# Performance work log

Hardware: AMD Instinct MI355X
Metric: run time of the kernel (lower is better)

Reference implementation:

```python
import jax, jax.numpy as jnp
import numpy as np

D_MODEL = 128; N_HEADS = 8; N_LEVELS = 1; N_POINTS = 8
MAX_RES = 10.0
B, H_SP, W_SP = 8, 64, 64


def setup_inputs() -> dict:
    key = jax.random.key(0)
    ks = jax.random.split(key, 8)
    s = 0.02
    f32 = jnp.float32
    return {
        "nbr_fea": jax.random.normal(ks[0], (B, D_MODEL, H_SP, W_SP), f32),
        "ext_fea": jax.random.normal(ks[1], (B, D_MODEL, H_SP, W_SP), f32),
        "W_val": jax.random.normal(ks[2], (D_MODEL, D_MODEL), f32) * s,
        "b_val": jnp.zeros((D_MODEL,), f32),
        "W_off": jax.random.normal(ks[3], (D_MODEL, N_HEADS * N_LEVELS * N_POINTS * 2), f32) * s,
        "b_off": jax.random.normal(ks[4], (N_HEADS * N_LEVELS * N_POINTS * 2,), f32) * s,
        "W_attn": jax.random.normal(ks[5], (D_MODEL, N_HEADS * N_LEVELS * N_POINTS), f32) * s,
        "b_attn": jnp.zeros((N_HEADS * N_LEVELS * N_POINTS,), f32),
        "W_out": jax.random.normal(ks[6], (D_MODEL, D_MODEL), f32) * s,
        "b_out": jnp.zeros((D_MODEL,), f32),
    }


def _deform_attn_align(nbr_fea, ext_fea, W_val, b_val, W_off, b_off, W_attn, b_attn, W_out, b_out):
    b, c, h, w = nbr_fea.shape
    L = h * w
    dh = c // N_HEADS
    # flatten b c h w -> b (h w) c
    query = jnp.transpose(ext_fea, (0, 2, 3, 1)).reshape(b, L, c)
    vin = jnp.transpose(nbr_fea, (0, 2, 3, 1)).reshape(b, L, c)

    # value projection (mask is all-False -> no masked fill needed)
    value = (vin @ W_val + b_val).reshape(b, L, N_HEADS, dh)
    vh = jnp.transpose(value, (0, 2, 1, 3))  # [b, H, L, dh]

    # sampling offsets, clamped by max_residue_magnitude * tanh
    off = MAX_RES * jnp.tanh(query @ W_off + b_off)
    off = off.reshape(b, L, N_HEADS, N_POINTS, 2)  # single level
    attn = jax.nn.softmax((query @ W_attn + b_attn).reshape(b, L, N_HEADS, N_POINTS), axis=-1)

    # reference points in [0,1]; valid_ratio == 1 since padding mask is all-False
    yy, xx = jnp.meshgrid(jnp.arange(h, dtype=jnp.float32), jnp.arange(w, dtype=jnp.float32), indexing="ij")
    ref = jnp.stack([(xx.reshape(-1) + 0.5) / w, (yy.reshape(-1) + 0.5) / h], axis=-1)  # [L, 2]
    norm = jnp.array([w, h], jnp.float32)  # offset_normalizer [W, H]
    loc = ref[None, :, None, None, :] + off / norm  # [b, L, H, P, 2]

    # grid_sample(align_corners=False, padding_mode='zeros') pixel coordinates
    px = jnp.transpose(loc[..., 0] * w - 0.5, (0, 2, 1, 3))  # [b, H, L, P]
    py = jnp.transpose(loc[..., 1] * h - 0.5, (0, 2, 1, 3))

    x0 = jnp.floor(px); y0 = jnp.floor(py)
    fx = px - x0; fy = py - y0
    x0i = x0.astype(jnp.int32); y0i = y0.astype(jnp.int32)

    def gather(xi, yi):
        valid = (xi >= 0) & (xi < w) & (yi >= 0) & (yi < h)
        idx = jnp.clip(yi, 0, h - 1) * w + jnp.clip(xi, 0, w - 1)  # [b, H, L, P]
        g = jnp.take_along_axis(vh, idx.reshape(b, N_HEADS, L * N_POINTS)[..., None], axis=2)
        return g.reshape(b, N_HEADS, L, N_POINTS, dh) * valid[..., None]

    samp = (gather(x0i, y0i) * ((1.0 - fx) * (1.0 - fy))[..., None]
            + gather(x0i + 1, y0i) * (fx * (1.0 - fy))[..., None]
            + gather(x0i, y0i + 1) * ((1.0 - fx) * fy)[..., None]
            + gather(x0i + 1, y0i + 1) * (fx * fy)[..., None])  # [b, H, L, P, dh]

    aw = jnp.transpose(attn, (0, 2, 1, 3))  # [b, H, L, P]
    out = jnp.sum(samp * aw[..., None], axis=3)  # [b, H, L, dh]
    out = jnp.transpose(out, (0, 2, 1, 3)).reshape(b, L, c)
    out = out @ W_out + b_out
    return jnp.transpose(out.reshape(b, h, w, c), (0, 3, 1, 2))  # b c h w


def reference(nbr_fea, ext_fea, W_val, b_val, W_off, b_off, W_attn, b_attn, W_out, b_out):
    return _deform_attn_align(nbr_fea, ext_fea, W_val, b_val, W_off, b_off, W_attn, b_attn, W_out, b_out)
```

## Files before the change

kernel.cpp:

```cpp
#include <hip/hip_runtime.h>
#include <cstdint>

#define HB 8
#define CM 128
#define NHEAD 8
#define NPT 8
#define DHD 16
#define HS 64
#define WS 64
#define LTOT 4096
#define NQA 192

typedef float floatx4 __attribute__((ext_vector_type(4)));
typedef short bf16x8 __attribute__((ext_vector_type(8)));

__device__ __forceinline__ unsigned short f2bf_rne(float x) {
  unsigned u = __float_as_uint(x);
  return (unsigned short)((u + 0x7FFFu + ((u >> 16) & 1)) >> 16);
}
__device__ __forceinline__ void split_bf(float x, unsigned short& h, unsigned short& l) {
  unsigned u = __float_as_uint(x);
  h = (unsigned short)(u >> 16);
  float r = x - __uint_as_float(u & 0xFFFF0000u);
  l = (unsigned short)(__float_as_uint(r) >> 16);
}
__device__ __forceinline__ float fast_tanh(float x) {
  float e = __expf(2.0f * x);
  return 1.0f - 2.0f / (e + 1.0f);
}

__global__ __launch_bounds__(256) void prep(const float* __restrict__ Wv,
                                            const float* __restrict__ Wo,
                                            const float* __restrict__ Wa,
                                            const float* __restrict__ Ww,
                                            const float* __restrict__ bo,
                                            const float* __restrict__ ba,
                                            unsigned short* __restrict__ wf_val,
                                            unsigned short* __restrict__ wf_qa,
                                            unsigned short* __restrict__ wf_out,
                                            float* __restrict__ bias_qa) {
  const int gid = blockIdx.x * 256 + threadIdx.x;
  const int k4 = gid / 448;
  const int ng = gid - k4 * 448;

  const float* src;
  unsigned short* dst;
  int Nsrc, Nn, nd, n;
  if (ng < 128) {        src = Wv; dst = wf_val; Nsrc = 128; Nn = 128; n = ng;        nd = n; }
  else if (ng < 256) {   src = Wo; dst = wf_qa;  Nsrc = 128; Nn = 192; n = ng - 128;  nd = n; }
  else if (ng < 320) {   src = Wa; dst = wf_qa;  Nsrc = 64;  Nn = 192; n = ng - 256;  nd = n + 128; }
  else {                 src = Ww; dst = wf_out; Nsrc = 128; Nn = 128; n = ng - 320;  nd = n; }

  ushort4 hi, lo;
  split_bf(src[(k4 * 4 + 0) * Nsrc + n], hi.x, lo.x);
  split_bf(src[(k4 * 4 + 1) * Nsrc + n], hi.y, lo.y);
  split_bf(src[(k4 * 4 + 2) * Nsrc + n], hi.z, lo.z);
  split_bf(src[(k4 * 4 + 3) * Nsrc + n], hi.w, lo.w);
  const int off = (k4 >> 1) * Nn * 8 + nd * 8 + (k4 & 1) * 4;
  *(ushort4*)(dst + off) = hi;
  *(ushort4*)(dst + Nn * 128 + off) = lo;

  if (gid < 128) bias_qa[gid] = bo[gid];
  else if (gid < 192) bias_qa[gid] = ba[gid - 128];
}

template <int N, int AMODE, int OUT_MODE>
__global__ __launch_bounds__(256, 4) void gemm_mfma(const void* __restrict__ Av,
                                                    const unsigned short* __restrict__ WF,
                                                    const float* __restrict__ bias,
                                                    float* __restrict__ out) {
  __shared__ char smem[32768];
  unsigned short* AB = (unsigned short*)smem;
  const int t = threadIdx.x;
  const int ml0 = blockIdx.x * 64;
  const int nb0 = blockIdx.y * 64;
  const int b = blockIdx.z;
  const int w = t >> 6, lane = t & 63;
  const int wm = (w >> 1) * 32, wn = (w & 1) * 32;
  const int nl = lane & 15, q = lane >> 4;

  bf16x8 wh[2][4], wl[2][4];
#pragma unroll
  for (int nt = 0; nt < 2; nt++) {
    const int n = nb0 + wn + nt * 16 + nl;
#pragma unroll
    for (int K0 = 0; K0 < 4; K0++) {
      const size_t o = (size_t)(K0 * 4 + q) * N * 8 + n * 8;
      wh[nt][K0] = *(const bf16x8*)(WF + o);
      wl[nt][K0] = *(const bf16x8*)(WF + (size_t)N * 128 + o);
    }
  }

  if (AMODE == 0) {
    const float* src = (const float*)Av + (size_t)b * CM * LTOT + ml0;
    const int x = t & 63, kq = t >> 6;
#pragma unroll
    for (int i = 0; i < 8; i++) {
      const int kb = kq * 4 + i * 16;
      ushort4 hi, lo;
      split_bf(src[(size_t)(kb + 0) * LTOT + x], hi.x, lo.x);
      split_bf(src[(size_t)(kb + 1) * LTOT + x], hi.y, lo.y);
      split_bf(src[(size_t)(kb + 2) * LTOT + x], hi.z, lo.z);
      split_bf(src[(size_t)(kb + 3) * LTOT + x], hi.w, lo.w);
      const int off = x * 128 + (((kb >> 3) ^ (x & 15)) << 3) + (kb & 7);
      *(ushort4*)(AB + off) = hi;
      *(ushort4*)(AB + 8192 + off) = lo;
    }
  } else {
    const unsigned short* src = (const unsigned short*)Av + ((size_t)b * LTOT + ml0) * CM;
#pragma unroll
    for (int i = 0; i < 4; i++) {
      const int idx = t + i * 256;
      const int x = idx >> 4, kc = idx & 15;
      const uint4 v = *(const uint4*)(src + (size_t)x * CM + kc * 8);
      *(uint4*)(AB + x * 128 + ((kc ^ (x & 15)) << 3)) = v;
    }
  }
  __syncthreads();

  floatx4 acc[2][2];
#pragma unroll
  for (int mt = 0; mt < 2; mt++)
#pragma unroll
    for (int nt = 0; nt < 2; nt++) acc[mt][nt] = {0.0f, 0.0f, 0.0f, 0.0f};

#pragma unroll
  for (int K0 = 0; K0 < 4; K0++) {
    bf16x8 ah[2], al[2];
#pragma unroll
    for (int mt = 0; mt < 2; mt++) {
      const int m = wm + mt * 16 + nl;
      const int off = m * 128 + (((K0 * 4 + q) ^ (m & 15)) << 3);
      ah[mt] = *(bf16x8*)(AB + off);
      if (AMODE == 0) al[mt] = *(bf16x8*)(AB + 8192 + off);
    }
#pragma unroll
    for (int mt = 0; mt < 2; mt++)
#pragma unroll
      for (int nt = 0; nt < 2; nt++) {
        if (AMODE == 0)
          acc[mt][nt] = __builtin_amdgcn_mfma_f32_16x16x32_bf16(al[mt], wh[nt][K0], acc[mt][nt], 0, 0, 0);
        acc[mt][nt] = __builtin_amdgcn_mfma_f32_16x16x32_bf16(ah[mt], wl[nt][K0], acc[mt][nt], 0, 0, 0);
        acc[mt][nt] = __builtin_amdgcn_mfma_f32_16x16x32_bf16(ah[mt], wh[nt][K0], acc[mt][nt], 0, 0, 0);
      }
  }

  if (OUT_MODE == 2) {
    __syncthreads();
    float* LF = (float*)smem;
#pragma unroll
    for (int mt = 0; mt < 2; mt++)
#pragma unroll
      for (int nt = 0; nt < 2; nt++) {
        const int n = wn + nt * 16 + nl;
#pragma unroll
        for (int r = 0; r < 4; r++) LF[n * 65 + wm + mt * 16 + q * 4 + r] = acc[mt][nt][r];
      }
    __syncthreads();
#pragma unroll
    for (int i = 0; i < 16; i++) {
      const int idx = t + i * 256;
      const int n = idx >> 6, m = idx & 63;
      out[((size_t)b * CM + nb0 + n) * LTOT + ml0 + m] = LF[n * 65 + m] + bias[nb0 + n];
    }
  } else {
#pragma unroll
    for (int nt = 0; nt < 2; nt++) {
      const int gc = nb0 + wn + nt * 16 + nl;
      const float bv = bias[gc];
#pragma unroll
      for (int mt = 0; mt < 2; mt++)
#pragma unroll
        for (int r = 0; r < 4; r++) {
          const int m = ml0 + wm + mt * 16 + q * 4 + r;
          const float v = acc[mt][nt][r] + bv;
          if (OUT_MODE == 0)
            out[(((size_t)b * NHEAD + (gc >> 4)) * LTOT + m) * DHD + (gc & 15)] = v;
          else
            out[((size_t)b * LTOT + m) * N + gc] = v;
        }
    }
  }
}

__global__ __launch_bounds__(256) void sampler(const float* __restrict__ value,
                                               const float* __restrict__ qa,
                                               unsigned short* __restrict__ attout) {
  const int t = threadIdx.x;
  const int lane = t & 63;
  const int w = t >> 6;
  const int d4 = lane & 3;
  const int p = (lane >> 2) & 7;
  const int li = lane >> 5;
  const int h = blockIdx.y;
  const int b = blockIdx.z;
  const int l = blockIdx.x * 8 + w * 2 + li;
  const size_t bl = (size_t)b * LTOT + l;

  const float2 off2 = *(const float2*)(qa + bl * NQA + h * 16 + p * 2);
  const float logit = qa[bl * NQA + 128 + h * 8 + p];

  float m = logit;
  m = fmaxf(m, __shfl_xor(m, 4));
  m = fmaxf(m, __shfl_xor(m, 8));
  m = fmaxf(m, __shfl_xor(m, 16));
  const float e = __expf(logit - m);
  float s = e;
  s += __shfl_xor(s, 4);
  s += __shfl_xor(s, 8);
  s += __shfl_xor(s, 16);
  const float aw = e / s;

  const float px = (float)(l & (WS - 1)) + 10.0f * fast_tanh(off2.x);
  const float py = (float)(l >> 6) + 10.0f * fast_tanh(off2.y);
  const float x0f = floorf(px), y0f = floorf(py);
  const float fx = px - x0f, fy = py - y0f;
  const int ix = (int)x0f, iy = (int)y0f;

  const float* vb = value + ((size_t)b * NHEAD + h) * (LTOT * DHD) + d4 * 4;
  float4 o = {0.0f, 0.0f, 0.0f, 0.0f};
#pragma unroll
  for (int c = 0; c < 4; c++) {
    const int cdx = c & 1, cdy = c >> 1;
    const int jx = ix + cdx, jy = iy + cdy;
    const float wx = cdx ? fx : 1.0f - fx;
    const float wy = cdy ? fy : 1.0f - fy;
    const bool valid = ((unsigned)jx < WS) & ((unsigned)jy < HS);
    const float wc = valid ? aw * wx * wy : 0.0f;
    const int cx = min(max(jx, 0), WS - 1);
    const int cy = min(max(jy, 0), HS - 1);
    const float4 v = *(const float4*)(vb + (size_t)((cy << 6) + cx) * DHD);
    o.x += wc * v.x;
    o.y += wc * v.y;
    o.z += wc * v.z;
    o.w += wc * v.w;
  }

  o.x += __shfl_xor(o.x, 4);  o.y += __shfl_xor(o.y, 4);
  o.z += __shfl_xor(o.z, 4);  o.w += __shfl_xor(o.w, 4);
  o.x += __shfl_xor(o.x, 8);  o.y += __shfl_xor(o.y, 8);
  o.z += __shfl_xor(o.z, 8);  o.w += __shfl_xor(o.w, 8);
  o.x += __shfl_xor(o.x, 16); o.y += __shfl_xor(o.y, 16);
  o.z += __shfl_xor(o.z, 16); o.w += __shfl_xor(o.w, 16);

  if (p == 0) {
    ushort4 st = {f2bf_rne(o.x), f2bf_rne(o.y), f2bf_rne(o.z), f2bf_rne(o.w)};
    *(ushort4*)(attout + bl * CM + h * 16 + d4 * 4) = st;
  }
}

extern "C" void kernel_launch(void* const* d_in, const int* in_sizes, int n_in,
                              void* d_out, int out_size, void* d_ws, size_t ws_size,
                              hipStream_t stream) {
  const float* nbr    = (const float*)d_in[0];
  const float* ext    = (const float*)d_in[1];
  const float* W_val  = (const float*)d_in[2];
  const float* b_val  = (const float*)d_in[3];
  const float* W_off  = (const float*)d_in[4];
  const float* b_off  = (const float*)d_in[5];
  const float* W_attn = (const float*)d_in[6];
  const float* b_attn = (const float*)d_in[7];
  const float* W_out  = (const float*)d_in[8];
  const float* b_out  = (const float*)d_in[9];
  float* out = (float*)d_out;

  float* value = (float*)d_ws;
  float* qa    = value + (size_t)HB * NHEAD * LTOT * DHD;
  unsigned short* attbf = (unsigned short*)(qa + (size_t)HB * LTOT * NQA);
  unsigned short* wf_val = attbf + (size_t)HB * LTOT * CM;
  unsigned short* wf_qa  = wf_val + 128 * 128 * 2;
  unsigned short* wf_out = wf_qa + 192 * 128 * 2;
  float* bias_qa = (float*)(wf_out + 128 * 128 * 2);

  prep<<<56, 256, 0, stream>>>(W_val, W_off, W_attn, W_out, b_off, b_attn,
                               wf_val, wf_qa, wf_out, bias_qa);
  gemm_mfma<128, 0, 0><<<dim3(64, 2, HB), 256, 0, stream>>>(nbr, wf_val, b_val, value);
  gemm_mfma<192, 0, 1><<<dim3(64, 3, HB), 256, 0, stream>>>(ext, wf_qa, bias_qa, qa);
  sampler<<<dim3(LTOT / 8, NHEAD, HB), 256, 0, stream>>>(value, qa, attbf);
  gemm_mfma<128, 2, 2><<<dim3(64, 2, HB), 256, 0, stream>>>(attbf, wf_out, b_out, out);
}
```

Measured before the change: 157.3 us.

## Merge value and query GEMM launches, batch sampler rows per warp, load weights per K-step

The value-projection and offset/attention-projection GEMMs now share one launch, with blockIdx.y choosing which body to run. This removes a kernel launch and lets the two GEMMs fill the GPU together. The sampler now has each warp handle four row pairs, with all qa loads issued up front so they overlap, and launches 4x fewer blocks. The GEMM now loads weight fragments inside the K loop instead of preloading all of them, which lowers register pressure but adds global loads in the inner loop.

Result: faster. 148.6 us (-5.6%).

```diff
diff --git a/kernel.cpp b/kernel.cpp
--- a/kernel.cpp
+++ b/kernel.cpp
@@ -65,31 +65,15 @@
 }
 
 template <int N, int AMODE, int OUT_MODE>
-__global__ __launch_bounds__(256, 4) void gemm_mfma(const void* __restrict__ Av,
-                                                    const unsigned short* __restrict__ WF,
-                                                    const float* __restrict__ bias,
-                                                    float* __restrict__ out) {
-  __shared__ char smem[32768];
+__device__ __forceinline__ void gemm_body(const void* __restrict__ Av,
+                                          const unsigned short* __restrict__ WF,
+                                          const float* __restrict__ bias,
+                                          float* __restrict__ out,
+                                          int b, int ml0, int nb0, int t, char* smem) {
   unsigned short* AB = (unsigned short*)smem;
-  const int t = threadIdx.x;
-  const int ml0 = blockIdx.x * 64;
-  const int nb0 = blockIdx.y * 64;
-  const int b = blockIdx.z;
   const int w = t >> 6, lane = t & 63;
   const int wm = (w >> 1) * 32, wn = (w & 1) * 32;
   const int nl = lane & 15, q = lane >> 4;
-
-  bf16x8 wh[2][4], wl[2][4];
-#pragma unroll
-  for (int nt = 0; nt < 2; nt++) {
-    const int n = nb0 + wn + nt * 16 + nl;
-#pragma unroll
-    for (int K0 = 0; K0 < 4; K0++) {
-      const size_t o = (size_t)(K0 * 4 + q) * N * 8 + n * 8;
-      wh[nt][K0] = *(const bf16x8*)(WF + o);
-      wl[nt][K0] = *(const bf16x8*)(WF + (size_t)N * 128 + o);
-    }
-  }
 
   if (AMODE == 0) {
     const float* src = (const float*)Av + (size_t)b * CM * LTOT + ml0;
@@ -134,14 +118,22 @@
       ah[mt] = *(bf16x8*)(AB + off);
       if (AMODE == 0) al[mt] = *(bf16x8*)(AB + 8192 + off);
     }
+    bf16x8 wh[2], wl[2];
+#pragma unroll
+    for (int nt = 0; nt < 2; nt++) {
+      const int n = nb0 + wn + nt * 16 + nl;
+      const size_t o = (size_t)(K0 * 4 + q) * N * 8 + n * 8;
+      wh[nt] = *(const bf16x8*)(WF + o);
+      wl[nt] = *(const bf16x8*)(WF + (size_t)N * 128 + o);
+    }
 #pragma unroll
     for (int mt = 0; mt < 2; mt++)
 #pragma unroll
       for (int nt = 0; nt < 2; nt++) {
         if (AMODE == 0)
-          acc[mt][nt] = __builtin_amdgcn_mfma_f32_16x16x32_bf16(al[mt], wh[nt][K0], acc[mt][nt], 0, 0, 0);
-        acc[mt][nt] = __builtin_amdgcn_mfma_f32_16x16x32_bf16(ah[mt], wl[nt][K0], acc[mt][nt], 0, 0, 0);
-        acc[mt][nt] = __builtin_amdgcn_mfma_f32_16x16x32_bf16(ah[mt], wh[nt][K0], acc[mt][nt], 0, 0, 0);
+          acc[mt][nt] = __builtin_amdgcn_mfma_f32_16x16x32_bf16(al[mt], wh[nt], acc[mt][nt], 0, 0, 0);
+        acc[mt][nt] = __builtin_amdgcn_mfma_f32_16x16x32_bf16(ah[mt], wl[nt], acc[mt][nt], 0, 0, 0);
+        acc[mt][nt] = __builtin_amdgcn_mfma_f32_16x16x32_bf16(ah[mt], wh[nt], acc[mt][nt], 0, 0, 0);
       }
   }
 
@@ -181,6 +173,31 @@
         }
     }
   }
+}
+
+__global__ __launch_bounds__(256, 4) void gemm_vq(const float* __restrict__ nbr,
+                                                  const float* __restrict__ ext,
+                                                  const unsigned short* __restrict__ wf_val,
+                                                  const unsigned short* __restrict__ wf_qa,
+                                                  const float* __restrict__ b_val,
+                                                  const float* __restrict__ bias_qa,
+                                                  float* __restrict__ value,
+                                                  float* __restrict__ qa) {
+  __shared__ char smem[32768];
+  const int b = blockIdx.z, ml0 = blockIdx.x * 64;
+  if (blockIdx.y < 2)
+    gemm_body<128, 0, 0>(nbr, wf_val, b_val, value, b, ml0, blockIdx.y * 64, threadIdx.x, smem);
+  else
+    gemm_body<192, 0, 1>(ext, wf_qa, bias_qa, qa, b, ml0, (blockIdx.y - 2) * 64, threadIdx.x, smem);
+}
+
+__global__ __launch_bounds__(256, 4) void gemm_outk(const unsigned short* __restrict__ attbf,
+                                                    const unsigned short* __restrict__ wf_out,
+                                                    const float* __restrict__ b_out,
+                                                    float* __restrict__ out) {
+  __shared__ char smem[32768];
+  gemm_body<128, 2, 2>(attbf, wf_out, b_out, out, blockIdx.z, blockIdx.x * 64,
+                       blockIdx.y * 64, threadIdx.x, smem);
 }
 
 __global__ __launch_bounds__(256) void sampler(const float* __restrict__ value,
@@ -194,58 +211,70 @@
   const int li = lane >> 5;
   const int h = blockIdx.y;
   const int b = blockIdx.z;
-  const int l = blockIdx.x * 8 + w * 2 + li;
-  const size_t bl = (size_t)b * LTOT + l;
-
-  const float2 off2 = *(const float2*)(qa + bl * NQA + h * 16 + p * 2);
-  const float logit = qa[bl * NQA + 128 + h * 8 + p];
-
-  float m = logit;
-  m = fmaxf(m, __shfl_xor(m, 4));
-  m = fmaxf(m, __shfl_xor(m, 8));
-  m = fmaxf(m, __shfl_xor(m, 16));
-  const float e = __expf(logit - m);
-  float s = e;
-  s += __shfl_xor(s, 4);
-  s += __shfl_xor(s, 8);
-  s += __shfl_xor(s, 16);
-  const float aw = e / s;
-
-  const float px = (float)(l & (WS - 1)) + 10.0f * fast_tanh(off2.x);
-  const float py = (float)(l >> 6) + 10.0f * fast_tanh(off2.y);
-  const float x0f = floorf(px), y0f = floorf(py);
-  const float fx = px - x0f, fy = py - y0f;
-  const int ix = (int)x0f, iy = (int)y0f;
+  const int l0 = blockIdx.x * 32 + w * 8;
+
+  float2 off2[4];
+  float lg[4];
+#pragma unroll
+  for (int it = 0; it < 4; it++) {
+    const size_t bl = (size_t)b * LTOT + l0 + it * 2 + li;
+    off2[it] = *(const float2*)(qa + bl * NQA + h * 16 + p * 2);
+    lg[it] = qa[bl * NQA + 128 + h * 8 + p];
+  }
 
   const float* vb = value + ((size_t)b * NHEAD + h) * (LTOT * DHD) + d4 * 4;
-  float4 o = {0.0f, 0.0f, 0.0f, 0.0f};
-#pragma unroll
-  for (int c = 0; c < 4; c++) {
-    const int cdx = c & 1, cdy = c >> 1;
-    const int jx = ix + cdx, jy = iy + cdy;
-    const float wx = cdx ? fx : 1.0f - fx;
-    const float wy = cdy ? fy : 1.0f - fy;
-    const bool valid = ((unsigned)jx < WS) & ((unsigned)jy < HS);
-    const float wc = valid ? aw * wx * wy : 0.0f;
-    const int cx = min(max(jx, 0), WS - 1);
-    const int cy = min(max(jy, 0), HS - 1);
-    const float4 v = *(const float4*)(vb + (size_t)((cy << 6) + cx) * DHD);
-    o.x += wc * v.x;
-    o.y += wc * v.y;
-    o.z += wc * v.z;
-    o.w += wc * v.w;
-  }
-
-  o.x += __shfl_xor(o.x, 4);  o.y += __shfl_xor(o.y, 4);
-  o.z += __shfl_xor(o.z, 4);  o.w += __shfl_xor(o.w, 4);
-  o.x += __shfl_xor(o.x, 8);  o.y += __shfl_xor(o.y, 8);
-  o.z += __shfl_xor(o.z, 8);  o.w += __shfl_xor(o.w, 8);
-  o.x += __shfl_xor(o.x, 16); o.y += __shfl_xor(o.y, 16);
-  o.z += __shfl_xor(o.z, 16); o.w += __shfl_xor(o.w, 16);
-
-  if (p == 0) {
-    ushort4 st = {f2bf_rne(o.x), f2bf_rne(o.y), f2bf_rne(o.z), f2bf_rne(o.w)};
-    *(ushort4*)(attout + bl * CM + h * 16 + d4 * 4) = st;
+
+#pragma unroll
+  for (int it = 0; it < 4; it++) {
+    const int l = l0 + it * 2 + li;
+    const size_t bl = (size_t)b * LTOT + l;
+
+    float m = lg[it];
+    m = fmaxf(m, __shfl_xor(m, 4));
+    m = fmaxf(m, __shfl_xor(m, 8));
+    m = fmaxf(m, __shfl_xor(m, 16));
+    const float e = __expf(lg[it] - m);
+    float s = e;
+    s += __shfl_xor(s, 4);
+    s += __shfl_xor(s, 8);
+    s += __shfl_xor(s, 16);
+    const float aw = e / s;
+
+    const float px = (float)(l & (WS - 1)) + 10.0f * fast_tanh(off2[it].x);
+    const float py = (float)(l >> 6) + 10.0f * fast_tanh(off2[it].y);
+    const float x0f = floorf(px), y0f = floorf(py);
+    const float fx = px - x0f, fy = py - y0f;
+    const int ix = (int)x0f, iy = (int)y0f;
+
+    float4 o = {0.0f, 0.0f, 0.0f, 0.0f};
+#pragma unroll
+    for (int c = 0; c < 4; c++) {
+      const int cdx = c & 1, cdy = c >> 1;
+      const int jx = ix + cdx, jy = iy + cdy;
+      const float wx = cdx ? fx : 1.0f - fx;
+      const float wy = cdy ? fy : 1.0f - fy;
+      const bool valid = ((unsigned)jx < WS) & ((unsigned)jy < HS);
+      const float wc = valid ? aw * wx * wy : 0.0f;
+      const int cx = min(max(jx, 0), WS - 1);
+      const int cy = min(max(jy, 0), HS - 1);
+      const float4 v = *(const float4*)(vb + (size_t)((cy << 6) + cx) * DHD);
+      o.x += wc * v.x;
+      o.y += wc * v.y;
+      o.z += wc * v.z;
+      o.w += wc * v.w;
+    }
+
+    o.x += __shfl_xor(o.x, 4);  o.y += __shfl_xor(o.y, 4);
+    o.z += __shfl_xor(o.z, 4);  o.w += __shfl_xor(o.w, 4);
+    o.x += __shfl_xor(o.x, 8);  o.y += __shfl_xor(o.y, 8);
+    o.z += __shfl_xor(o.z, 8);  o.w += __shfl_xor(o.w, 8);
+    o.x += __shfl_xor(o.x, 16); o.y += __shfl_xor(o.y, 16);
+    o.z += __shfl_xor(o.z, 16); o.w += __shfl_xor(o.w, 16);
+
+    if (p == 0) {
+      ushort4 st = {f2bf_rne(o.x), f2bf_rne(o.y), f2bf_rne(o.z), f2bf_rne(o.w)};
+      *(ushort4*)(attout + bl * CM + h * 16 + d4 * 4) = st;
+    }
   }
 }
 
@@ -274,8 +303,7 @@
 
   prep<<<56, 256, 0, stream>>>(W_val, W_off, W_attn, W_out, b_off, b_attn,
                                wf_val, wf_qa, wf_out, bias_qa);
-  gemm_mfma<128, 0, 0><<<dim3(64, 2, HB), 256, 0, stream>>>(nbr, wf_val, b_val, value);
-  gemm_mfma<192, 0, 1><<<dim3(64, 3, HB), 256, 0, stream>>>(ext, wf_qa, bias_qa, qa);
-  sampler<<<dim3(LTOT / 8, NHEAD, HB), 256, 0, stream>>>(value, qa, attbf);
-  gemm_mfma<128, 2, 2><<<dim3(64, 2, HB), 256, 0, stream>>>(attbf, wf_out, b_out, out);
-}
+  gemm_vq<<<dim3(64, 5, HB), 256, 0, stream>>>(nbr, ext, wf_val, wf_qa, b_val, bias_qa, value, qa);
+  sampler<<<dim3(LTOT / 32, NHEAD, HB), 256, 0, stream>>>(value, qa, attbf);
+  gemm_outk<<<dim3(64, 2, HB), 256, 0, stream>>>(attbf, wf_out, b_out, out);
+}
```

## Fuse value/query GEMMs into one launch and fuse sampler with output projection

Applied to the files above, without the earlier changes.

Merges the value and offset/attention projection GEMMs into a single kernel, where each block computes the full N width for a 64-row tile so the fp32-to-split-bf16 A conversion is done once per tile rather than once per N-block. The bilinear sampler is fused with the output projection: each block samples a 64-position tile for all heads into LDS as bf16, then multiplies it by W_out with MFMA. This removes the bf16 intermediate round trip through global memory and two kernel launches. The cost is fewer, larger blocks (512 blocks for sampling plus output) with per-thread serial loops over 8 points, so less parallelism and latency hiding in the gather phase.

Result: no change. 158.1 us (+0.5%).

```diff
diff --git a/kernel.cpp b/kernel.cpp
--- a/kernel.cpp
+++ b/kernel.cpp
@@ -64,35 +64,17 @@
   else if (gid < 192) bias_qa[gid] = ba[gid - 128];
 }
 
-template <int N, int AMODE, int OUT_MODE>
-__global__ __launch_bounds__(256, 4) void gemm_mfma(const void* __restrict__ Av,
-                                                    const unsigned short* __restrict__ WF,
-                                                    const float* __restrict__ bias,
-                                                    float* __restrict__ out) {
-  __shared__ char smem[32768];
+template <int N, int OUT_MODE>
+__device__ __forceinline__ void gemm_wide(const float* __restrict__ A,
+                                          const unsigned short* __restrict__ WF,
+                                          const float* __restrict__ bias,
+                                          float* __restrict__ out,
+                                          int b, int ml0, int t, char* smem) {
+  constexpr int NT = N / 32;
   unsigned short* AB = (unsigned short*)smem;
-  const int t = threadIdx.x;
-  const int ml0 = blockIdx.x * 64;
-  const int nb0 = blockIdx.y * 64;
-  const int b = blockIdx.z;
-  const int w = t >> 6, lane = t & 63;
-  const int wm = (w >> 1) * 32, wn = (w & 1) * 32;
-  const int nl = lane & 15, q = lane >> 4;
-
-  bf16x8 wh[2][4], wl[2][4];
-#pragma unroll
-  for (int nt = 0; nt < 2; nt++) {
-    const int n = nb0 + wn + nt * 16 + nl;
-#pragma unroll
-    for (int K0 = 0; K0 < 4; K0++) {
-      const size_t o = (size_t)(K0 * 4 + q) * N * 8 + n * 8;
-      wh[nt][K0] = *(const bf16x8*)(WF + o);
-      wl[nt][K0] = *(const bf16x8*)(WF + (size_t)N * 128 + o);
-    }
-  }
-
-  if (AMODE == 0) {
-    const float* src = (const float*)Av + (size_t)b * CM * LTOT + ml0;
+
+  {
+    const float* src = A + (size_t)b * CM * LTOT + ml0;
     const int x = t & 63, kq = t >> 6;
 #pragma unroll
     for (int i = 0; i < 8; i++) {
@@ -106,23 +88,18 @@
       *(ushort4*)(AB + off) = hi;
       *(ushort4*)(AB + 8192 + off) = lo;
     }
-  } else {
-    const unsigned short* src = (const unsigned short*)Av + ((size_t)b * LTOT + ml0) * CM;
-#pragma unroll
-    for (int i = 0; i < 4; i++) {
-      const int idx = t + i * 256;
-      const int x = idx >> 4, kc = idx & 15;
-      const uint4 v = *(const uint4*)(src + (size_t)x * CM + kc * 8);
-      *(uint4*)(AB + x * 128 + ((kc ^ (x & 15)) << 3)) = v;
-    }
   }
   __syncthreads();
 
-  floatx4 acc[2][2];
+  const int w = t >> 6, lane = t & 63;
+  const int wm = (w >> 1) * 32, wn = (w & 1) * (N / 2);
+  const int nl = lane & 15, q = lane >> 4;
+
+  floatx4 acc[2][NT];
 #pragma unroll
   for (int mt = 0; mt < 2; mt++)
 #pragma unroll
-    for (int nt = 0; nt < 2; nt++) acc[mt][nt] = {0.0f, 0.0f, 0.0f, 0.0f};
+    for (int j = 0; j < NT; j++) acc[mt][j] = {0.0f, 0.0f, 0.0f, 0.0f};
 
 #pragma unroll
   for (int K0 = 0; K0 < 4; K0++) {
@@ -132,120 +109,172 @@
       const int m = wm + mt * 16 + nl;
       const int off = m * 128 + (((K0 * 4 + q) ^ (m & 15)) << 3);
       ah[mt] = *(bf16x8*)(AB + off);
-      if (AMODE == 0) al[mt] = *(bf16x8*)(AB + 8192 + off);
-    }
+      al[mt] = *(bf16x8*)(AB + 8192 + off);
+    }
+#pragma unroll
+    for (int j = 0; j < NT; j++) {
+      const int n = wn + j * 16 + nl;
+      const size_t o = (size_t)(K0 * 4 + q) * N * 8 + n * 8;
+      const bf16x8 wh = *(const bf16x8*)(WF + o);
+      const bf16x8 wl = *(const bf16x8*)(WF + (size_t)N * 128 + o);
+#pragma unroll
+      for (int mt = 0; mt < 2; mt++) {
+        acc[mt][j] = __builtin_amdgcn_mfma_f32_16x16x32_bf16(al[mt], wh, acc[mt][j], 0, 0, 0);
+        acc[mt][j] = __builtin_amdgcn_mfma_f32_16x16x32_bf16(ah[mt], wl, acc[mt][j], 0, 0, 0);
+        acc[mt][j] = __builtin_amdgcn_mfma_f32_16x16x32_bf16(ah[mt], wh, acc[mt][j], 0, 0, 0);
+      }
+    }
+  }
+
+#pragma unroll
+  for (int j = 0; j < NT; j++) {
+    const int gc = wn + j * 16 + nl;
+    const float bv = bias[gc];
 #pragma unroll
     for (int mt = 0; mt < 2; mt++)
 #pragma unroll
-      for (int nt = 0; nt < 2; nt++) {
-        if (AMODE == 0)
-          acc[mt][nt] = __builtin_amdgcn_mfma_f32_16x16x32_bf16(al[mt], wh[nt][K0], acc[mt][nt], 0, 0, 0);
-        acc[mt][nt] = __builtin_amdgcn_mfma_f32_16x16x32_bf16(ah[mt], wl[nt][K0], acc[mt][nt], 0, 0, 0);
-        acc[mt][nt] = __builtin_amdgcn_mfma_f32_16x16x32_bf16(ah[mt], wh[nt][K0], acc[mt][nt], 0, 0, 0);
+      for (int r = 0; r < 4; r++) {
+        const int m = ml0 + wm + mt * 16 + q * 4 + r;
+        const float v = acc[mt][j][r] + bv;
+        if (OUT_MODE == 0)
+          out[(((size_t)b * NHEAD + (gc >> 4)) * LTOT + m) * DHD + (gc & 15)] = v;
+        else
+          out[((size_t)b * LTOT + m) * NQA + gc] = v;
       }
   }
-
-  if (OUT_MODE == 2) {
-    __syncthreads();
-    float* LF = (float*)smem;
-#pragma unroll
-    for (int mt = 0; mt < 2; mt++)
-#pragma unroll
-      for (int nt = 0; nt < 2; nt++) {
-        const int n = wn + nt * 16 + nl;
-#pragma unroll
-        for (int r = 0; r < 4; r++) LF[n * 65 + wm + mt * 16 + q * 4 + r] = acc[mt][nt][r];
+}
+
+__global__ __launch_bounds__(256, 4) void gemm_vq(const float* __restrict__ nbr,
+                                                  const float* __restrict__ ext,
+                                                  const unsigned short* __restrict__ wf_val,
+                                                  const unsigned short* __restrict__ wf_qa,
+                                                  const float* __restrict__ b_val,
+                                                  const float* __restrict__ bias_qa,
+                                                  float* __restrict__ value,
+                                                  float* __restrict__ qa) {
+  __shared__ char smem[32768];
+  if (blockIdx.y == 0)
+    gemm_wide<128, 0>(nbr, wf_val, b_val, value, blockIdx.z, blockIdx.x * 64, threadIdx.x, smem);
+  else
+    gemm_wide<192, 1>(ext, wf_qa, bias_qa, qa, blockIdx.z, blockIdx.x * 64, threadIdx.x, smem);
+}
+
+__global__ __launch_bounds__(512, 2) void samp_out(const float* __restrict__ value,
+                                                   const float* __restrict__ qa,
+                                                   const unsigned short* __restrict__ wf_out,
+                                                   const float* __restrict__ b_out,
+                                                   float* __restrict__ out) {
+  __shared__ char smem[33280];
+  unsigned short* FR = (unsigned short*)smem;
+  const int t = threadIdx.x;
+  const int b = blockIdx.y;
+  const int ml0 = blockIdx.x * 64;
+  const int d4 = t & 3;
+  const int u = t >> 2;
+
+#pragma unroll
+  for (int ps = 0; ps < 4; ps++) {
+    const int idx = ps * 128 + u;
+    const int ll = idx >> 3;
+    const int h = idx & 7;
+    const int l = ml0 + ll;
+    const size_t bl = (size_t)b * LTOT + l;
+    const float* qrow = qa + bl * NQA;
+
+    float4 of[4];
+#pragma unroll
+    for (int j = 0; j < 4; j++) of[j] = *(const float4*)(qrow + h * 16 + j * 4);
+    const float4 lga = *(const float4*)(qrow + 128 + h * 8);
+    const float4 lgb = *(const float4*)(qrow + 128 + h * 8 + 4);
+    float lg[8] = {lga.x, lga.y, lga.z, lga.w, lgb.x, lgb.y, lgb.z, lgb.w};
+
+    float m = lg[0];
+#pragma unroll
+    for (int p = 1; p < 8; p++) m = fmaxf(m, lg[p]);
+    float e[8], s = 0.0f;
+#pragma unroll
+    for (int p = 0; p < 8; p++) { e[p] = __expf(lg[p] - m); s += e[p]; }
+    const float inv = 1.0f / s;
+
+    const float xf = (float)(l & (WS - 1));
+    const float yf = (float)(l >> 6);
+    const float* vb = value + ((size_t)b * NHEAD + h) * (LTOT * DHD) + d4 * 4;
+
+    float4 o = {0.0f, 0.0f, 0.0f, 0.0f};
+#pragma unroll
+    for (int p = 0; p < 8; p++) {
+      const float ox = (p & 1) ? of[p >> 1].z : of[p >> 1].x;
+      const float oy = (p & 1) ? of[p >> 1].w : of[p >> 1].y;
+      const float aw = e[p] * inv;
+      const float px = xf + 10.0f * fast_tanh(ox);
+      const float py = yf + 10.0f * fast_tanh(oy);
+      const float x0f = floorf(px), y0f = floorf(py);
+      const float fx = px - x0f, fy = py - y0f;
+      const int ix = (int)x0f, iy = (int)y0f;
+#pragma unroll
+      for (int c = 0; c < 4; c++) {
+        const int cdx = c & 1, cdy = c >> 1;
+        const int jx = ix + cdx, jy = iy + cdy;
+        const float wx = cdx ? fx : 1.0f - fx;
+        const float wy = cdy ? fy : 1.0f - fy;
+        const bool valid = ((unsigned)jx < WS) & ((unsigned)jy < HS);
+        const float wc = valid ? aw * wx * wy : 0.0f;
+        const int cx = min(max(jx, 0), WS - 1);
+        const int cy = min(max(jy, 0), HS - 1);
+        const float4 v = *(const float4*)(vb + (size_t)((cy << 6) + cx) * DHD);
+        o.x += wc * v.x;
+        o.y += wc * v.y;
+        o.z += wc * v.z;
+        o.w += wc * v.w;
       }
-    __syncthreads();
-#pragma unroll
-    for (int i = 0; i < 16; i++) {
-      const int idx = t + i * 256;
-      const int n = idx >> 6, m = idx & 63;
-      out[((size_t)b * CM + nb0 + n) * LTOT + ml0 + m] = LF[n * 65 + m] + bias[nb0 + n];
-    }
-  } else {
-#pragma unroll
-    for (int nt = 0; nt < 2; nt++) {
-      const int gc = nb0 + wn + nt * 16 + nl;
-      const float bv = bias[gc];
-#pragma unroll
-      for (int mt = 0; mt < 2; mt++)
-#pragma unroll
-        for (int r = 0; r < 4; r++) {
-          const int m = ml0 + wm + mt * 16 + q * 4 + r;
-          const float v = acc[mt][nt][r] + bv;
-          if (OUT_MODE == 0)
-            out[(((size_t)b * NHEAD + (gc >> 4)) * LTOT + m) * DHD + (gc & 15)] = v;
-          else
-            out[((size_t)b * LTOT + m) * N + gc] = v;
-        }
-    }
-  }
-}
-
-__global__ __launch_bounds__(256) void sampler(const float* __restrict__ value,
-                                               const float* __restrict__ qa,
-                                               unsigned short* __restrict__ attout) {
-  const int t = threadIdx.x;
-  const int lane = t & 63;
-  const int w = t >> 6;
-  const int d4 = lane & 3;
-  const int p = (lane >> 2) & 7;
-  const int li = lane >> 5;
-  const int h = blockIdx.y;
-  const int b = blockIdx.z;
-  const int l = blockIdx.x * 8 + w * 2 + li;
-  const size_t bl = (size_t)b * LTOT + l;
-
-  const float2 off2 = *(const float2*)(qa + bl * NQA + h * 16 + p * 2);
-  const float logit = qa[bl * NQA + 128 + h * 8 + p];
-
-  float m = logit;
-  m = fmaxf(m, __shfl_xor(m, 4));
-  m = fmaxf(m, __shfl_xor(m, 8));
-  m = fmaxf(m, __shfl_xor(m, 16));
-  const float e = __expf(logit - m);
-  float s = e;
-  s += __shfl_xor(s, 4);
-  s += __shfl_xor(s, 8);
-  s += __shfl_xor(s, 16);
-  const float aw = e / s;
-
-  const float px = (float)(l & (WS - 1)) + 10.0f * fast_tanh(off2.x);
-  const float py = (float)(l >> 6) + 10.0f * fast_tanh(off2.y);
-  const float x0f = floorf(px), y0f = floorf(py);
-  const float fx = px - x0f, fy = py - y0f;
-  const int ix = (int)x0f, iy = (int)y0f;
-
-  const float* vb = value + ((size_t)b * NHEAD + h) * (LTOT * DHD) + d4 * 4;
-  float4 o = {0.0f, 0.0f, 0.0f, 0.0f};
-#pragma unroll
-  for (int c = 0; c < 4; c++) {
-    const int cdx = c & 1, cdy = c >> 1;
-    const int jx = ix + cdx, jy = iy + cdy;
-    const float wx = cdx ? fx : 1.0f - fx;
-    const float wy = cdy ? fy : 1.0f - fy;
-    const bool valid = ((unsigned)jx < WS) & ((unsigned)jy < HS);
-    const float wc = valid ? aw * wx * wy : 0.0f;
-    const int cx = min(max(jx, 0), WS - 1);
-    const int cy = min(max(jy, 0), HS - 1);
-    const float4 v = *(const float4*)(vb + (size_t)((cy << 6) + cx) * DHD);
-    o.x += wc * v.x;
-    o.y += wc * v.y;
-    o.z += wc * v.z;
-    o.w += wc * v.w;
-  }
-
-  o.x += __shfl_xor(o.x, 4);  o.y += __shfl_xor(o.y, 4);
-  o.z += __shfl_xor(o.z, 4);  o.w += __shfl_xor(o.w, 4);
-  o.x += __shfl_xor(o.x, 8);  o.y += __shfl_xor(o.y, 8);
-  o.z += __shfl_xor(o.z, 8);  o.w += __shfl_xor(o.w, 8);
-  o.x += __shfl_xor(o.x, 16); o.y += __shfl_xor(o.y, 16);
-  o.z += __shfl_xor(o.z, 16); o.w += __shfl_xor(o.w, 16);
-
-  if (p == 0) {
+    }
+
+    const int off = ll * 128 + (((h * 2 + (d4 >> 1)) ^ (ll & 15)) << 3) + (d4 & 1) * 4;
     ushort4 st = {f2bf_rne(o.x), f2bf_rne(o.y), f2bf_rne(o.z), f2bf_rne(o.w)};
-    *(ushort4*)(attout + bl * CM + h * 16 + d4 * 4) = st;
+    *(ushort4*)(FR + off) = st;
+  }
+  __syncthreads();
+
+  const int w = t >> 6, lane = t & 63;
+  const int nl = lane & 15, q = lane >> 4;
+  const int wm = (w >> 1) * 16;
+  const int wn = (w & 1) * 64;
+
+  floatx4 acc[4];
+#pragma unroll
+  for (int j = 0; j < 4; j++) acc[j] = {0.0f, 0.0f, 0.0f, 0.0f};
+
+#pragma unroll
+  for (int K0 = 0; K0 < 4; K0++) {
+    const int m = wm + nl;
+    const int off = m * 128 + (((K0 * 4 + q) ^ (m & 15)) << 3);
+    const bf16x8 ah = *(bf16x8*)(FR + off);
+#pragma unroll
+    for (int j = 0; j < 4; j++) {
+      const int n = wn + j * 16 + nl;
+      const size_t o = (size_t)(K0 * 4 + q) * CM * 8 + n * 8;
+      const bf16x8 wh = *(const bf16x8*)(wf_out + o);
+      const bf16x8 wl = *(const bf16x8*)(wf_out + (size_t)CM * 128 + o);
+      acc[j] = __builtin_amdgcn_mfma_f32_16x16x32_bf16(ah, wl, acc[j], 0, 0, 0);
+      acc[j] = __builtin_amdgcn_mfma_f32_16x16x32_bf16(ah, wh, acc[j], 0, 0, 0);
+    }
+  }
+
+  __syncthreads();
+  float* LF = (float*)smem;
+#pragma unroll
+  for (int j = 0; j < 4; j++) {
+    const int n = wn + j * 16 + nl;
+#pragma unroll
+    for (int r = 0; r < 4; r++) LF[n * 65 + wm + q * 4 + r] = acc[j][r];
+  }
+  __syncthreads();
+
+#pragma unroll
+  for (int i = 0; i < 16; i++) {
+    const int idx = t + i * 512;
+    const int n = idx >> 6, m = idx & 63;
+    out[((size_t)b * CM + n) * LTOT + ml0 + m] = LF[n * 65 + m] + b_out[n];
   }
 }
 
@@ -266,16 +295,13 @@
 
   float* value = (float*)d_ws;
   float* qa    = value + (size_t)HB * NHEAD * LTOT * DHD;
-  unsigned short* attbf = (unsigned short*)(qa + (size_t)HB * LTOT * NQA);
-  unsigned short* wf_val = attbf + (size_t)HB * LTOT * CM;
+  unsigned short* wf_val = (unsigned short*)(qa + (size_t)HB * LTOT * NQA);
   unsigned short* wf_qa  = wf_val + 128 * 128 * 2;
   unsigned short* wf_out = wf_qa + 192 * 128 * 2;
   float* bias_qa = (float*)(wf_out + 128 * 128 * 2);
 
   prep<<<56, 256, 0, stream>>>(W_val, W_off, W_attn, W_out, b_off, b_attn,
                                wf_val, wf_qa, wf_out, bias_qa);
-  gemm_mfma<128, 0, 0><<<dim3(64, 2, HB), 256, 0, stream>>>(nbr, wf_val, b_val, value);
-  gemm_mfma<192, 0, 1><<<dim3(64, 3, HB), 256, 0, stream>>>(ext, wf_qa, bias_qa, qa);
-  sampler<<<dim3(LTOT / 8, NHEAD, HB), 256, 0, stream>>>(value, qa, attbf);
-  gemm_mfma<128, 2, 2><<<dim3(64, 2, HB), 256, 0, stream>>>(attbf, wf_out, b_out, out);
-}
+  gemm_vq<<<dim3(64, 2, HB), 256, 0, stream>>>(nbr, ext, wf_val, wf_qa, b_val, bias_qa, value, qa);
+  samp_out<<<dim3(64, HB), 512, 0, stream>>>(value, qa, wf_out, b_out, out);
+}
```
